# Performance work log

Hardware: AMD Instinct MI355X
Metric: run time of the kernel (lower is better)

Reference implementation:

```python
import jax, jax.numpy as jnp
import numpy as np

N_CLUSTERS = 2048
MAX_ITER = 5


def setup_inputs() -> dict:
    key = jax.random.key(0)
    k1, k2 = jax.random.split(key)
    X = jax.random.normal(k1, (131072, 128), dtype=jnp.float32)
    init_centroids = jax.random.normal(k2, (N_CLUSTERS, 128), dtype=jnp.float32)
    return {"X": X, "init_centroids": init_centroids}


def _euc_sim(a, b):
    # 2 a.b^T - |a|^2 - |b|^2  (negative squared euclidean distance)
    return (2.0 * (a @ b.T)
            - jnp.sum(a * a, axis=1)[:, None]
            - jnp.sum(b * b, axis=1)[None, :])


def reference(X, init_centroids):
    K = init_centroids.shape[0]

    def step(centroids, _):
        sim = _euc_sim(X, centroids)              # [N, K]
        closest = jnp.argmax(sim, axis=-1)         # [N]
        sums = jax.ops.segment_sum(X, closest, num_segments=K)        # [K, d]
        counts = jax.ops.segment_sum(jnp.ones_like(closest, dtype=X.dtype),
                                     closest, num_segments=K)         # [K]
        # full-batch branch: c_grad = mask @ x / mask.sum(-1), NaN -> 0
        c_grad = jnp.where(counts[:, None] > 0, sums / jnp.maximum(counts, 1.0)[:, None], 0.0)
        # minibatch is None => lr = 1 => centroids <- c_grad
        return c_grad, closest

    centroids, closest_hist = jax.lax.scan(step, init_centroids, None, length=MAX_ITER)
    labels = closest_hist[-1]
    return centroids, labels
```

## Files before the change

kernel.cpp:

```cpp
#include <hip/hip_runtime.h>
#include <hip/hip_bf16.h>

#define NP 131072
#define D 128
#define KC 2048
#define ITERS 5
#define CG 8

#define TAU 0.03f

#if defined(__has_builtin)
#if __has_builtin(__builtin_amdgcn_global_load_lds)
#define USE_GLL 1
#endif
#endif

typedef short bf16x8 __attribute__((ext_vector_type(8)));
typedef float f32x4 __attribute__((ext_vector_type(4)));

__device__ inline unsigned short f2bf(float x) {
    __hip_bfloat16 b = __float2bfloat16(x);
    return *reinterpret_cast<unsigned short*>(&b);
}
__device__ inline float bf2f(unsigned short u) {
    union { unsigned int i; float f; } c; c.i = ((unsigned int)u) << 16; return c.f;
}

__device__ inline size_t pslot(int k, int d, int hl) {
    int g = k >> 4, t15 = k & 15, ks = d >> 5, q = (d >> 3) & 3, e = d & 7;
    return ((size_t)((ks * 128 + g) * 2 + hl)) * 512 + (q * 16 + t15) * 8 + e;
}

__global__ void init_kernel(const float* __restrict__ initC,
                            double* __restrict__ C64, double* __restrict__ CT64,
                            unsigned short* __restrict__ Pn) {
    int t = blockIdx.x * 256 + threadIdx.x;
    float v = initC[t];
    C64[t] = (double)v;
    CT64[(size_t)(t & 127) * KC + (t >> 7)] = (double)v;
    unsigned short h = f2bf(v);
    int k = t >> 7, d = t & 127;
    Pn[pslot(k, d, 0)] = h;
    Pn[pslot(k, d, 1)] = f2bf(v - bf2f(h));
}

__global__ void cnorm_kernel(const double* __restrict__ C64,
                             double* __restrict__ n64, float* __restrict__ n32,
                             int* __restrict__ counter) {
    int r = blockIdx.x * 4 + (threadIdx.x >> 6);
    int lane = threadIdx.x & 63;
    double a = C64[(size_t)r * D + lane * 2];
    double b = C64[(size_t)r * D + lane * 2 + 1];
    double s = a * a + b * b;
#pragma unroll
    for (int m = 1; m < 64; m <<= 1) s += __shfl_xor(s, m, 64);
    if (lane == 0) { n64[r] = s; n32[r] = (float)s; }
    if (blockIdx.x == 0 && threadIdx.x == 0) *counter = 0;
}

__global__ __launch_bounds__(256, 4)
void assign_kernel(const float* __restrict__ X,
                   const unsigned short* __restrict__ Pn,
                   const float* __restrict__ cnorm,
                   int* __restrict__ labels,
                   int* __restrict__ list,
                   int* __restrict__ counter) {
    __shared__ __align__(16) char lds[32768];

    const int tid = threadIdx.x;
    const int lane = tid & 63;
    const int wid = tid >> 6;
    const int wrow = wid >> 1;
    const int wcol = wid & 1;
    const int t15 = lane & 15;
    const int q = lane >> 4;
    const int pbase = blockIdx.x * 64;

#pragma unroll
    for (int i = 0; i < 8; i++) {
        int f = i * 256 + tid;
        int row = f >> 5, c4 = f & 31;
        float4 v = *(const float4*)&X[(size_t)(pbase + row) * D + c4 * 4];
        unsigned short h0 = f2bf(v.x), h1 = f2bf(v.y), h2 = f2bf(v.z), h3 = f2bf(v.w);
        unsigned short l0 = f2bf(v.x - bf2f(h0)), l1 = f2bf(v.y - bf2f(h1));
        unsigned short l2 = f2bf(v.z - bf2f(h2)), l3 = f2bf(v.w - bf2f(h3));
        uint2 ph = { (unsigned)h0 | ((unsigned)h1 << 16), (unsigned)h2 | ((unsigned)h3 << 16) };
        uint2 pl = { (unsigned)l0 | ((unsigned)l1 << 16), (unsigned)l2 | ((unsigned)l3 << 16) };
        int ad = (row * 256 + c4 * 8) ^ ((row & 7) << 4);
        *(uint2*)(lds + ad) = ph;
        *(uint2*)(lds + 16384 + ad) = pl;
    }
    __syncthreads();

    bf16x8 rah[2][4], ral[2][4];
#pragma unroll
    for (int rt = 0; rt < 2; rt++) {
        int row = wrow * 32 + rt * 16 + t15;
        int sw = (row & 7) << 4;
#pragma unroll
        for (int ks = 0; ks < 4; ks++) {
            int ad = (row * 256 + ks * 64 + q * 16) ^ sw;
            rah[rt][ks] = *(const bf16x8*)(lds + ad);
            ral[rt][ks] = *(const bf16x8*)(lds + 16384 + ad);
        }
    }
    __syncthreads();

    float b1[8], b2[8];
    int i1[8];
#pragma unroll
    for (int s = 0; s < 8; s++) { b1[s] = -INFINITY; b2[s] = -INFINITY; i1[s] = 0x7fffffff; }

    const char* PnB = (const char*)Pn;

#pragma unroll
    for (int i = 0; i < 4; i++) {
        int seg = wid * 4 + i;
        const char* src = PnB + seg * 1024;
#if USE_GLL
        __builtin_amdgcn_global_load_lds(
            (const __attribute__((address_space(1))) unsigned int*)(src + lane * 16),
            (__attribute__((address_space(3))) unsigned int*)(lds + seg * 1024),
            16, 0, 0);
#else
        uint4 v = *(const uint4*)(src + lane * 16);
        *(uint4*)(lds + seg * 1024 + lane * 16) = v;
#endif
    }
    __syncthreads();

    for (int ct = 0; ct < KC / 128; ct++) {
        f32x4 acc[2][4];
#pragma unroll
        for (int rt = 0; rt < 2; rt++)
#pragma unroll
            for (int cj = 0; cj < 4; cj++) acc[rt][cj] = (f32x4){0.f, 0.f, 0.f, 0.f};

#pragma unroll
        for (int ks = 0; ks < 4; ks++) {
            const int cur = (ct * 4 + ks) & 1;
            char* bcur = lds + cur * 16384;
            char* bnext = lds + (cur ^ 1) * 16384;

            const int nct = (ks == 3) ? ((ct < 15) ? ct + 1 : 15) : ct;
            const int nks = (ks + 1) & 3;
            const char* nsrc = PnB + ((size_t)(nks * 128 + nct * 8)) * 2048;
#pragma unroll
            for (int i = 0; i < 4; i++) {
                int seg = wid * 4 + i;
#if USE_GLL
                __builtin_amdgcn_global_load_lds(
                    (const __attribute__((address_space(1))) unsigned int*)(nsrc + seg * 1024 + lane * 16),
                    (__attribute__((address_space(3))) unsigned int*)(bnext + seg * 1024),
                    16, 0, 0);
#else
                uint4 v = *(const uint4*)(nsrc + seg * 1024 + lane * 16);
                *(uint4*)(bnext + seg * 1024 + lane * 16) = v;
#endif
            }

            __builtin_amdgcn_s_setprio(1);
#pragma unroll
            for (int cj = 0; cj < 4; cj++) {
                int gl = wcol * 4 + cj;
                bf16x8 bh = *(const bf16x8*)(bcur + gl * 2048 + lane * 16);
                bf16x8 bl = *(const bf16x8*)(bcur + gl * 2048 + 1024 + lane * 16);
#pragma unroll
                for (int rt = 0; rt < 2; rt++) {
                    acc[rt][cj] = __builtin_amdgcn_mfma_f32_16x16x32_bf16(rah[rt][ks], bh, acc[rt][cj], 0, 0, 0);
                    acc[rt][cj] = __builtin_amdgcn_mfma_f32_16x16x32_bf16(rah[rt][ks], bl, acc[rt][cj], 0, 0, 0);
                    acc[rt][cj] = __builtin_amdgcn_mfma_f32_16x16x32_bf16(ral[rt][ks], bh, acc[rt][cj], 0, 0, 0);
                }
            }
            __builtin_amdgcn_s_setprio(0);
            __syncthreads();
        }

#pragma unroll
        for (int cj = 0; cj < 4; cj++) {
            int col = ct * 128 + wcol * 64 + cj * 16 + t15;
            float cnv = cnorm[col];
#pragma unroll
            for (int rt = 0; rt < 2; rt++)
#pragma unroll
                for (int rg = 0; rg < 4; rg++) {
                    int s = rt * 4 + rg;
                    float sv = __builtin_fmaf(2.0f, acc[rt][cj][rg], -cnv);
                    bool gt1 = sv > b1[s];
                    float mx2 = fmaxf(b2[s], sv);
                    b2[s] = gt1 ? b1[s] : mx2;
                    i1[s] = gt1 ? col : i1[s];
                    b1[s] = gt1 ? sv : b1[s];
                }
        }
    }

#pragma unroll
    for (int s = 0; s < 8; s++) {
#pragma unroll
        for (int m = 1; m < 16; m <<= 1) {
            float ob1 = __shfl_xor(b1[s], m, 64);
            int   oi  = __shfl_xor(i1[s], m, 64);
            float ob2 = __shfl_xor(b2[s], m, 64);
            bool gt = ob1 > b1[s];
            bool eq = ob1 == b1[s];
            float nb2 = gt ? fmaxf(b1[s], ob2) : fmaxf(b2[s], ob1);
            nb2 = eq ? b1[s] : nb2;
            int ni = gt ? oi : i1[s];
            ni = (eq && oi < i1[s]) ? oi : ni;
            b1[s] = gt ? ob1 : b1[s];
            b2[s] = nb2;
            i1[s] = ni;
        }
    }

    __syncthreads();
    float* mb1 = (float*)lds;
    float* mb2 = ((float*)lds) + 128;
    int*   mi1 = (int*)(((float*)lds) + 256);
    if (t15 == 0) {
#pragma unroll
        for (int rt = 0; rt < 2; rt++)
#pragma unroll
            for (int rg = 0; rg < 4; rg++) {
                int s = rt * 4 + rg;
                int row = wrow * 32 + rt * 16 + q * 4 + rg;
                mb1[wcol * 64 + row] = b1[s];
                mb2[wcol * 64 + row] = b2[s];
                mi1[wcol * 64 + row] = i1[s];
            }
    }
    __syncthreads();
    if (tid < 64) {
        float a1 = mb1[tid], a2 = mb2[tid];  int ai = mi1[tid];
        float c1 = mb1[64 + tid], c2 = mb2[64 + tid];  int ci = mi1[64 + tid];
        float best, second;  int bi;
        if (a1 > c1)      { best = a1; bi = ai; second = fmaxf(a2, c1); }
        else if (a1 < c1) { best = c1; bi = ci; second = fmaxf(c2, a1); }
        else              { best = a1; bi = (ai < ci) ? ai : ci; second = a1; }
        int p = pbase + tid;
        labels[p] = bi;
        if (best - second < TAU) {
            int idx = atomicAdd(counter, 1);
            list[idx] = p;
        }
    }
}

__global__ void recheck_kernel(const float* __restrict__ X,
                               const double* __restrict__ CT64,
                               const double* __restrict__ cn64,
                               const int* __restrict__ list,
                               const int* __restrict__ counter,
                               int* __restrict__ labels) {
    __shared__ float xrow[D];
    __shared__ double rb[4];
    __shared__ int ri[4];
    int cnt = *counter;
    for (int ii = blockIdx.x; ii < cnt; ii += gridDim.x) {
        int p = list[ii];
        __syncthreads();
        if (threadIdx.x < D) xrow[threadIdx.x] = X[(size_t)p * D + threadIdx.x];
        __syncthreads();
        double xn = 0.0;
#pragma unroll 16
        for (int d = 0; d < D; d++) {
            double xv = (double)xrow[d];
            xn = fma(xv, xv, xn);
        }
        double best = -1.0e300;
        int bi = 0x7fffffff;
#pragma unroll
        for (int g = 0; g < 8; g++) {
            int c = threadIdx.x + 256 * g;
            double acc = 0.0;
#pragma unroll 16
            for (int d = 0; d < D; d++)
                acc = fma((double)xrow[d], CT64[(size_t)d * KC + c], acc);
            double s = 2.0 * acc - xn - cn64[c];
            if (s > best || (s == best && c < bi)) { best = s; bi = c; }
        }
#pragma unroll
        for (int m = 1; m < 64; m <<= 1) {
            double ob = __shfl_xor(best, m, 64);
            int oi = __shfl_xor(bi, m, 64);
            if (ob > best || (ob == best && oi < bi)) { best = ob; bi = oi; }
        }
        int w = threadIdx.x >> 6;
        if ((threadIdx.x & 63) == 0) { rb[w] = best; ri[w] = bi; }
        __syncthreads();
        if (threadIdx.x == 0) {
            double bb = rb[0]; int bbi = ri[0];
            for (int w2 = 1; w2 < 4; w2++)
                if (rb[w2] > bb || (rb[w2] == bb && ri[w2] < bbi)) { bb = rb[w2]; bbi = ri[w2]; }
            labels[p] = bbi;
        }
    }
}

__global__ __launch_bounds__(512)
void accum_kernel(const float* __restrict__ X,
                  const int* __restrict__ labels,
                  double* __restrict__ sums,
                  int* __restrict__ counts) {
    __shared__ double sred[8][CG][64][2];
    __shared__ int cred[8][CG];
    const int lane = threadIdx.x & 63;
    const int w = threadIdx.x >> 6;
    const int kbase = blockIdx.x * CG;
    const int base0 = w * (NP / 8);
    double s0[CG], s1[CG];
    int cnt[CG];
#pragma unroll
    for (int c = 0; c < CG; c++) { s0[c] = 0.0; s1[c] = 0.0; cnt[c] = 0; }

    for (int it = 0; it < (NP / 8) / 256; it++) {
        int4 lab = *(const int4*)&labels[base0 + it * 256 + lane * 4];
#pragma unroll
        for (int j = 0; j < 4; j++) {
            int lv = (j == 0) ? lab.x : (j == 1) ? lab.y : (j == 2) ? lab.z : lab.w;
            int rel = lv - kbase;
#pragma unroll
            for (int c = 0; c < CG; c++) {
                unsigned long long m = __ballot(rel == c);
                cnt[c] += __popcll(m);
                while (m) {
                    int b = __ffsll(m) - 1;
                    m &= m - 1;
                    int p = base0 + it * 256 + b * 4 + j;
                    float2 v = *(const float2*)&X[(size_t)p * D + lane * 2];
                    s0[c] += (double)v.x;
                    s1[c] += (double)v.y;
                }
            }
        }
    }
#pragma unroll
    for (int c = 0; c < CG; c++) {
        sred[w][c][lane][0] = s0[c];
        sred[w][c][lane][1] = s1[c];
    }
    if (lane < CG) cred[w][lane] = cnt[lane];
    __syncthreads();

#pragma unroll
    for (int rep = 0; rep < 2; rep++) {
        int idx = rep * 512 + threadIdx.x;
        int c = idx >> 7, d = idx & 127;
        double s = 0.0;
#pragma unroll
        for (int ww = 0; ww < 8; ww++) s += sred[ww][c][d >> 1][d & 1];
        sums[(size_t)(kbase + c) * D + d] = s;
    }
    if (threadIdx.x < CG) {
        int s = 0;
#pragma unroll
        for (int ww = 0; ww < 8; ww++) s += cred[ww][threadIdx.x];
        counts[kbase + threadIdx.x] = s;
    }
}

__global__ void update_kernel(const double* __restrict__ sums,
                              const int* __restrict__ counts,
                              double* __restrict__ C64, double* __restrict__ CT64,
                              unsigned short* __restrict__ Pn,
                              float* __restrict__ outC) {
    int t = blockIdx.x * 256 + threadIdx.x;
    int k = t >> 7;
    int n = counts[k];
    double v = (n > 0) ? sums[t] / (double)n : 0.0;
    C64[t] = v;
    CT64[(size_t)(t & 127) * KC + k] = v;
    float vf = (float)v;
    unsigned short h = f2bf(vf);
    int d = t & 127;
    Pn[pslot(k, d, 0)] = h;
    Pn[pslot(k, d, 1)] = f2bf(vf - bf2f(h));
    if (outC) outC[t] = vf;
}

__global__ void lab2f_kernel(const int* __restrict__ labels, float* __restrict__ out) {
    int t = blockIdx.x * 256 + threadIdx.x;
    out[t] = (float)labels[t];
}

extern "C" void kernel_launch(void* const* d_in, const int* in_sizes, int n_in,
                              void* d_out, int out_size, void* d_ws, size_t ws_size,
                              hipStream_t stream) {
    const float* X = (const float*)d_in[0];
    const float* initC = (const float*)d_in[1];
    float* out = (float*)d_out;

    char* w = (char*)d_ws;
    const size_t MB = 1u << 20;
    double* C64    = (double*)(w);
    double* S64    = (double*)(w + 2 * MB);
    double* CT64   = (double*)(w + 4 * MB);
    unsigned short* Pn = (unsigned short*)(w + 6 * MB);
    int*    labels = (int*)   (w + 7 * MB);
    int*    list   = (int*)   (w + 7 * MB + 512 * 1024);
    double* cn64   = (double*)(w + 8 * MB);
    float*  cn32   = (float*) (w + 8 * MB + 16 * 1024);
    int*    counts = (int*)   (w + 8 * MB + 24 * 1024);
    int*    counter= (int*)   (w + 8 * MB + 32 * 1024);

    init_kernel<<<(KC * D) / 256, 256, 0, stream>>>(initC, C64, CT64, Pn);

    for (int it = 0; it < ITERS; it++) {
        cnorm_kernel<<<KC / 4, 256, 0, stream>>>(C64, cn64, cn32, counter);
        assign_kernel<<<NP / 64, 256, 0, stream>>>(X, Pn, cn32, labels, list, counter);
        recheck_kernel<<<1024, 256, 0, stream>>>(X, CT64, cn64, list, counter, labels);
        accum_kernel<<<KC / CG, 512, 0, stream>>>(X, labels, S64, counts);
        update_kernel<<<(KC * D) / 256, 256, 0, stream>>>(
            S64, counts, C64, CT64, Pn, (it == ITERS - 1) ? out : nullptr);
    }
    lab2f_kernel<<<NP / 256, 256, 0, stream>>>(labels, out + (size_t)KC * D);
}
```

Before: 2.247 ms.

## Triple-buffer centroid tiles with explicit vmcnt waits and stage cnorm via LDS

Replaces the double-buffered centroid-panel loop in the assign kernel with a three-stage LDS ring, prefetching two steps ahead. Each step waits with a hand-set s_waitcnt vmcnt and a raw barrier instead of a full __syncthreads. Centroid norms for each tile are also loaded asynchronously into LDS rather than read from global memory in the epilogue. The goal is to hide global-to-LDS load latency behind MFMA work, at the cost of more LDS, occupancy lowered from 4 to 3 blocks, and fragile hand-counted vmcnt values.

```diff
diff --git a/kernel.cpp b/kernel.cpp
--- a/kernel.cpp
+++ b/kernel.cpp
@@ -8,6 +8,7 @@
 #define CG 8
 
 #define TAU 0.03f
+#define CNOFF 49152
 
 #if defined(__has_builtin)
 #if __has_builtin(__builtin_amdgcn_global_load_lds)
@@ -30,6 +31,18 @@
     int g = k >> 4, t15 = k & 15, ks = d >> 5, q = (d >> 3) & 3, e = d & 7;
     return ((size_t)((ks * 128 + g) * 2 + hl)) * 512 + (q * 16 + t15) * 8 + e;
 }
+
+#if USE_GLL
+#define GLL16(srcp, dstp) __builtin_amdgcn_global_load_lds( \
+    (const __attribute__((address_space(1))) unsigned int*)(srcp), \
+    (__attribute__((address_space(3))) unsigned int*)(dstp), 16, 0, 0)
+#define GLL4(srcp, dstp) __builtin_amdgcn_global_load_lds( \
+    (const __attribute__((address_space(1))) unsigned int*)(srcp), \
+    (__attribute__((address_space(3))) unsigned int*)(dstp), 4, 0, 0)
+#else
+#define GLL16(srcp, dstp) do { *(uint4*)((char*)(dstp) + lane * 16) = *(const uint4*)(srcp); } while (0)
+#define GLL4(srcp, dstp)  do { *(unsigned int*)((char*)(dstp) + lane * 4) = *(const unsigned int*)(srcp); } while (0)
+#endif
 
 __global__ void init_kernel(const float* __restrict__ initC,
                             double* __restrict__ C64, double* __restrict__ CT64,
@@ -58,14 +71,14 @@
     if (blockIdx.x == 0 && threadIdx.x == 0) *counter = 0;
 }
 
-__global__ __launch_bounds__(256, 4)
+__global__ __launch_bounds__(256, 3)
 void assign_kernel(const float* __restrict__ X,
                    const unsigned short* __restrict__ Pn,
                    const float* __restrict__ cnorm,
                    int* __restrict__ labels,
                    int* __restrict__ list,
                    int* __restrict__ counter) {
-    __shared__ __align__(16) char lds[32768];
+    __shared__ __align__(16) char lds[49664];
 
     const int tid = threadIdx.x;
     const int lane = tid & 63;
@@ -75,6 +88,7 @@
     const int t15 = lane & 15;
     const int q = lane >> 4;
     const int pbase = blockIdx.x * 64;
+    const char* PnB = (const char*)Pn;
 
 #pragma unroll
     for (int i = 0; i < 8; i++) {
@@ -111,23 +125,54 @@
 #pragma unroll
     for (int s = 0; s < 8; s++) { b1[s] = -INFINITY; b2[s] = -INFINITY; i1[s] = 0x7fffffff; }
 
-    const char* PnB = (const char*)Pn;
-
 #pragma unroll
     for (int i = 0; i < 4; i++) {
         int seg = wid * 4 + i;
-        const char* src = PnB + seg * 1024;
-#if USE_GLL
-        __builtin_amdgcn_global_load_lds(
-            (const __attribute__((address_space(1))) unsigned int*)(src + lane * 16),
-            (__attribute__((address_space(3))) unsigned int*)(lds + seg * 1024),
-            16, 0, 0);
-#else
-        uint4 v = *(const uint4*)(src + lane * 16);
-        *(uint4*)(lds + seg * 1024 + lane * 16) = v;
-#endif
-    }
-    __syncthreads();
+        GLL16(PnB + seg * 1024 + lane * 16, lds + seg * 1024);
+    }
+#pragma unroll
+    for (int i = 0; i < 4; i++) {
+        int seg = wid * 4 + i;
+        GLL16(PnB + (size_t)(1 * 128) * 2048 + seg * 1024 + lane * 16,
+              lds + 16384 + seg * 1024);
+    }
+
+#define STEP(KS, VMSTR) do {                                                  \
+        asm volatile("s_waitcnt vmcnt(" VMSTR ")" ::: "memory");              \
+        __builtin_amdgcn_s_barrier();                                         \
+        asm volatile("" ::: "memory");                                        \
+        __builtin_amdgcn_sched_barrier(0);                                    \
+        int t_ = ct * 4 + (KS);                                               \
+        int s2_ = t_ + 2;                                                     \
+        int s2c_ = (s2_ > 63) ? 63 : s2_;                                     \
+        char* bstage_ = lds + (unsigned)(s2_ % 3) * 16384;                    \
+        const char* nsrc_ = PnB + ((size_t)((s2c_ & 3) * 128 + (s2c_ >> 2) * 8)) * 2048; \
+        _Pragma("unroll")                                                     \
+        for (int i_ = 0; i_ < 4; i_++) {                                      \
+            int seg_ = wid * 4 + i_;                                          \
+            GLL16(nsrc_ + seg_ * 1024 + lane * 16, bstage_ + seg_ * 1024);    \
+        }                                                                     \
+        if ((KS) == 0) {                                                      \
+            const float* cs_ = cnorm + ct * 128;                              \
+            GLL4(cs_ + lane, lds + CNOFF);                                    \
+            GLL4(cs_ + 64 + lane, lds + CNOFF + 256);                         \
+        }                                                                     \
+        const char* bcur_ = lds + (unsigned)(t_ % 3) * 16384;                 \
+        __builtin_amdgcn_s_setprio(1);                                        \
+        _Pragma("unroll")                                                     \
+        for (int cj_ = 0; cj_ < 4; cj_++) {                                   \
+            int gl_ = wcol * 4 + cj_;                                         \
+            bf16x8 bh_ = *(const bf16x8*)(bcur_ + gl_ * 2048 + lane * 16);    \
+            bf16x8 bl_ = *(const bf16x8*)(bcur_ + gl_ * 2048 + 1024 + lane * 16); \
+            _Pragma("unroll")                                                 \
+            for (int rt_ = 0; rt_ < 2; rt_++) {                               \
+                acc[rt_][cj_] = __builtin_amdgcn_mfma_f32_16x16x32_bf16(rah[rt_][KS], bh_, acc[rt_][cj_], 0, 0, 0); \
+                acc[rt_][cj_] = __builtin_amdgcn_mfma_f32_16x16x32_bf16(rah[rt_][KS], bl_, acc[rt_][cj_], 0, 0, 0); \
+                acc[rt_][cj_] = __builtin_amdgcn_mfma_f32_16x16x32_bf16(ral[rt_][KS], bh_, acc[rt_][cj_], 0, 0, 0); \
+            }                                                                 \
+        }                                                                     \
+        __builtin_amdgcn_s_setprio(0);                                        \
+    } while (0)
 
     for (int ct = 0; ct < KC / 128; ct++) {
         f32x4 acc[2][4];
@@ -136,50 +181,16 @@
 #pragma unroll
             for (int cj = 0; cj < 4; cj++) acc[rt][cj] = (f32x4){0.f, 0.f, 0.f, 0.f};
 
-#pragma unroll
-        for (int ks = 0; ks < 4; ks++) {
-            const int cur = (ct * 4 + ks) & 1;
-            char* bcur = lds + cur * 16384;
-            char* bnext = lds + (cur ^ 1) * 16384;
-
-            const int nct = (ks == 3) ? ((ct < 15) ? ct + 1 : 15) : ct;
-            const int nks = (ks + 1) & 3;
-            const char* nsrc = PnB + ((size_t)(nks * 128 + nct * 8)) * 2048;
-#pragma unroll
-            for (int i = 0; i < 4; i++) {
-                int seg = wid * 4 + i;
-#if USE_GLL
-                __builtin_amdgcn_global_load_lds(
-                    (const __attribute__((address_space(1))) unsigned int*)(nsrc + seg * 1024 + lane * 16),
-                    (__attribute__((address_space(3))) unsigned int*)(bnext + seg * 1024),
-                    16, 0, 0);
-#else
-                uint4 v = *(const uint4*)(nsrc + seg * 1024 + lane * 16);
-                *(uint4*)(bnext + seg * 1024 + lane * 16) = v;
-#endif
-            }
-
-            __builtin_amdgcn_s_setprio(1);
-#pragma unroll
-            for (int cj = 0; cj < 4; cj++) {
-                int gl = wcol * 4 + cj;
-                bf16x8 bh = *(const bf16x8*)(bcur + gl * 2048 + lane * 16);
-                bf16x8 bl = *(const bf16x8*)(bcur + gl * 2048 + 1024 + lane * 16);
-#pragma unroll
-                for (int rt = 0; rt < 2; rt++) {
-                    acc[rt][cj] = __builtin_amdgcn_mfma_f32_16x16x32_bf16(rah[rt][ks], bh, acc[rt][cj], 0, 0, 0);
-                    acc[rt][cj] = __builtin_amdgcn_mfma_f32_16x16x32_bf16(rah[rt][ks], bl, acc[rt][cj], 0, 0, 0);
-                    acc[rt][cj] = __builtin_amdgcn_mfma_f32_16x16x32_bf16(ral[rt][ks], bh, acc[rt][cj], 0, 0, 0);
-                }
-            }
-            __builtin_amdgcn_s_setprio(0);
-            __syncthreads();
-        }
-
+        STEP(0, "4");
+        STEP(1, "6");
+        STEP(2, "6");
+        STEP(3, "4");
+
+        const float* cnL = (const float*)(lds + CNOFF);
 #pragma unroll
         for (int cj = 0; cj < 4; cj++) {
             int col = ct * 128 + wcol * 64 + cj * 16 + t15;
-            float cnv = cnorm[col];
+            float cnv = cnL[wcol * 64 + cj * 16 + t15];
 #pragma unroll
             for (int rt = 0; rt < 2; rt++)
 #pragma unroll
@@ -194,6 +205,7 @@
                 }
         }
     }
+#undef STEP
 
 #pragma unroll
     for (int s = 0; s < 8; s++) {
```

After: 2.080 ms. -7.5%, faster.
